# Kernel optimization log

Measured on AMD Instinct MI355X. Metric: run time of the kernel, lower is better.

## Reference

```python
import jax, jax.numpy as jnp
import numpy as np

N_NODES = 50000
N_EDGES = 640000
IN_CH, HID, OUT_CH = 128, 256, 3


def setup_inputs() -> dict:
    key = jax.random.key(0)
    ks = jax.random.split(key, 6)
    x = jax.random.normal(ks[0], (N_NODES, IN_CH), dtype=jnp.float32)
    edge_index = jax.random.randint(ks[1], (2, N_EDGES), 0, N_NODES, dtype=jnp.int64)
    # Glorot-ish scaling for weights
    Wl0 = jax.random.normal(ks[2], (IN_CH, HID), dtype=jnp.float32) / np.sqrt(IN_CH)
    bl0 = jnp.zeros((HID,), dtype=jnp.float32)
    Wr0 = jax.random.normal(ks[3], (IN_CH, HID), dtype=jnp.float32) / np.sqrt(IN_CH)
    Wl1 = jax.random.normal(ks[4], (HID, OUT_CH), dtype=jnp.float32) / np.sqrt(HID)
    bl1 = jnp.zeros((OUT_CH,), dtype=jnp.float32)
    Wr1 = jax.random.normal(ks[5], (HID, OUT_CH), dtype=jnp.float32) / np.sqrt(HID)
    return {"x": x, "edge_index": edge_index, "Wl0": Wl0, "bl0": bl0, "Wr0": Wr0,
            "Wl1": Wl1, "bl1": bl1, "Wr1": Wr1}


def _sage_conv(x, src, dst, Wl, bl, Wr, num_nodes):
    # mean aggregation of source features into destination nodes
    msg_sum = jax.ops.segment_sum(x[src], dst, num_segments=num_nodes)  # [N, d_in]
    deg = jax.ops.segment_sum(jnp.ones((src.shape[0],), x.dtype), dst, num_segments=num_nodes)
    mean = msg_sum / jnp.maximum(deg, 1.0)[:, None]
    # PyG SAGEConv: lin_l(aggr) + lin_r(x_self); lin_l carries the bias
    return mean @ Wl + bl + x @ Wr


def reference(x, edge_index, Wl0, bl0, Wr0, Wl1, bl1, Wr1):
    src, dst = edge_index[0], edge_index[1]
    h = _sage_conv(x, src, dst, Wl0, bl0, Wr0, N_NODES)
    h = jax.nn.relu(h)
    # dropout is identity in eval mode (training=False)
    return _sage_conv(h, src, dst, Wl1, bl1, Wr1, N_NODES)
```

## Files before the change

### kernel.cpp

```cpp
#include <hip/hip_runtime.h>

#define NN 50000
#define NNP 50048
#define NE 640000
#define IC 128
#define HC 256
#define OC 3

#define TOBF16_BLOCKS (NN * IC / 4 / 256)
#define WPACK_BLOCKS  32
#define ZERO_BLOCKS   ((NN + 1 + 255) / 256)

typedef __attribute__((ext_vector_type(8))) short short8;
typedef __attribute__((ext_vector_type(4))) float f32x4;

__device__ __forceinline__ unsigned short f2bf(float f) {
    unsigned int u = __float_as_uint(f);
    unsigned int r = u + 0x7FFFu + ((u >> 16) & 1u);
    return (unsigned short)(r >> 16);
}
__device__ __forceinline__ float bflo(unsigned int v) { return __uint_as_float(v << 16); }
__device__ __forceinline__ float bfhi(unsigned int v) { return __uint_as_float(v & 0xffff0000u); }

__global__ __launch_bounds__(256) void k_prep(const float* __restrict__ x,
                                              const float* __restrict__ Wl0,
                                              const float* __restrict__ Wr0,
                                              unsigned short* __restrict__ Ab,
                                              unsigned short* __restrict__ Bp,
                                              int* __restrict__ degi) {
    int b = blockIdx.x;
    int t = threadIdx.x;
    if (b < TOBF16_BLOCKS) {
        int i = b * 256 + t;
        int n = i >> 5;
        int c = (i & 31) * 4;
        float4 v = ((const float4*)x)[i];
        ushort4 o;
        o.x = f2bf(v.x); o.y = f2bf(v.y); o.z = f2bf(v.z); o.w = f2bf(v.w);
        *(ushort4*)&Ab[(size_t)n * 256 + 128 + c] = o;
    } else if (b < TOBF16_BLOCKS + WPACK_BLOCKS) {
        int tt = (b - TOBF16_BLOCKS) * 256 + t;
        int l = tt & 63;
        int nt = (tt >> 6) & 15;
        int kt = tt >> 10;
        int n = nt * 16 + (l & 15);
        int kbase = kt * 32 + (l >> 4) * 8;
        unsigned short o[8];
        #pragma unroll
        for (int e = 0; e < 8; ++e) {
            int k = kbase + e;
            float w = (k < IC) ? Wl0[k * HC + n] : Wr0[(k - IC) * HC + n];
            o[e] = f2bf(w);
        }
        #pragma unroll
        for (int e = 0; e < 8; ++e) Bp[(size_t)tt * 8 + e] = o[e];
    } else {
        int idx = (b - TOBF16_BLOCKS - WPACK_BLOCKS) * 256 + t;
        if (idx <= NN) degi[idx] = 0;
    }
}

__global__ __launch_bounds__(256) void k_deg(const int* __restrict__ ei,
                                             int* __restrict__ degi,
                                             int* __restrict__ pos) {
    int e = blockIdx.x * blockDim.x + threadIdx.x;
    if (e >= NE) return;
    pos[e] = atomicAdd(&degi[ei[NE + e]], 1);
}

__global__ __launch_bounds__(256) void k_ticket(const int* __restrict__ degi,
                                                int* __restrict__ counter,
                                                int* __restrict__ rowstart) {
    int n = blockIdx.x * blockDim.x + threadIdx.x;
    if (n >= NN) return;
    rowstart[n] = atomicAdd(counter, degi[n]);
}

__global__ __launch_bounds__(256) void k_fill(const int* __restrict__ ei,
                                              const int* __restrict__ rowstart,
                                              const int* __restrict__ pos,
                                              int* __restrict__ csr) {
    int e = blockIdx.x * blockDim.x + threadIdx.x;
    if (e >= NE) return;
    int src = ei[e];
    int dst = ei[NE + e];
    csr[rowstart[dst] + pos[e]] = src;
}

__global__ __launch_bounds__(256) void k_agg(const int* __restrict__ rowstart,
                                             const int* __restrict__ degi,
                                             const int* __restrict__ csr,
                                             unsigned short* __restrict__ Ab) {
    int wid = (blockIdx.x * blockDim.x + threadIdx.x) >> 6;
    int lane = threadIdx.x & 63;
    if (wid >= NN) return;
    int deg = degi[wid];
    int beg = rowstart[wid];
    int sg = lane >> 4;
    int s  = lane & 15;
    const uint4* base = (const uint4*)Ab;

    float a[8] = {0.f, 0.f, 0.f, 0.f, 0.f, 0.f, 0.f, 0.f};
    for (int j = beg + sg; j < beg + deg; j += 4) {
        int src = csr[j];
        uint4 v = base[(size_t)src * 32 + 16 + s];
        a[0] += bflo(v.x); a[1] += bfhi(v.x);
        a[2] += bflo(v.y); a[3] += bfhi(v.y);
        a[4] += bflo(v.z); a[5] += bfhi(v.z);
        a[6] += bflo(v.w); a[7] += bfhi(v.w);
    }
    #pragma unroll
    for (int m = 16; m <= 32; m <<= 1)
        #pragma unroll
        for (int i = 0; i < 8; ++i) a[i] += __shfl_xor(a[i], m);

    if (sg == 0) {
        float inv = 1.0f / fmaxf((float)deg, 1.0f);
        uint4 o;
        o.x = ((unsigned int)f2bf(a[1] * inv) << 16) | f2bf(a[0] * inv);
        o.y = ((unsigned int)f2bf(a[3] * inv) << 16) | f2bf(a[2] * inv);
        o.z = ((unsigned int)f2bf(a[5] * inv) << 16) | f2bf(a[4] * inv);
        o.w = ((unsigned int)f2bf(a[7] * inv) << 16) | f2bf(a[6] * inv);
        ((uint4*)Ab)[(size_t)wid * 32 + s] = o;
    }
}

__global__ __launch_bounds__(256) void k_gemm(const unsigned short* __restrict__ Ab,
                                              const unsigned short* __restrict__ Bp,
                                              const float* __restrict__ bl0,
                                              const float* __restrict__ Wl1,
                                              const float* __restrict__ Wr1,
                                              float* __restrict__ g,
                                              float* __restrict__ r) {
    __shared__ float4 Bs[2048];
    __shared__ float wl1s[HC][3];
    __shared__ float wr1s[HC][3];
    __shared__ float bls[HC];

    int t = threadIdx.x;
    for (int i = t; i < HC * 3; i += 256) {
        wl1s[i / 3][i % 3] = Wl1[i];
        wr1s[i / 3][i % 3] = Wr1[i];
    }
    for (int i = t; i < HC; i += 256) bls[i] = bl0[i];

    int w = t >> 6, l = t & 63;
    int n0 = blockIdx.x * 64 + w * 16;

    f32x4 acc[16];
    #pragma unroll
    for (int i = 0; i < 16; ++i) acc[i] = (f32x4){0.f, 0.f, 0.f, 0.f};

    const short8* A8 = (const short8*)Ab + ((size_t)(n0 + (l & 15)) * 32 + (l >> 4));

    for (int q = 0; q < 4; ++q) {
        __syncthreads();
        const float4* gsrc = (const float4*)(Bp + (size_t)q * 16384);
        #pragma unroll
        for (int i = 0; i < 8; ++i)
            Bs[i * 256 + t] = gsrc[i * 256 + t];
        __syncthreads();
        #pragma unroll
        for (int j = 0; j < 2; ++j) {
            int kt = q * 2 + j;
            short8 af = A8[kt * 4];
            const short8* B8 = (const short8*)Bs + (j * 1024 + l);
            #pragma unroll
            for (int nt = 0; nt < 16; ++nt) {
                short8 bf = B8[nt * 64];
                acc[nt] = __builtin_amdgcn_mfma_f32_16x16x32_bf16(af, bf, acc[nt], 0, 0, 0);
            }
        }
    }

    float pl[4][3] = {{0.f}}, pr[4][3] = {{0.f}};
    #pragma unroll
    for (int nt = 0; nt < 16; ++nt) {
        int col = nt * 16 + (l & 15);
        float b = bls[col];
        #pragma unroll
        for (int e = 0; e < 4; ++e) {
            float h = fmaxf(acc[nt][e] + b, 0.0f);
            #pragma unroll
            for (int j = 0; j < 3; ++j) {
                pl[e][j] = fmaf(h, wl1s[col][j], pl[e][j]);
                pr[e][j] = fmaf(h, wr1s[col][j], pr[e][j]);
            }
        }
    }
    #pragma unroll
    for (int m = 1; m <= 8; m <<= 1) {
        #pragma unroll
        for (int e = 0; e < 4; ++e)
            #pragma unroll
            for (int j = 0; j < 3; ++j) {
                pl[e][j] += __shfl_xor(pl[e][j], m);
                pr[e][j] += __shfl_xor(pr[e][j], m);
            }
    }
    if ((l & 15) == 0) {
        #pragma unroll
        for (int e = 0; e < 4; ++e) {
            int node = n0 + (l >> 4) * 4 + e;
            if (node < NN) {
                #pragma unroll
                for (int j = 0; j < 3; ++j) {
                    g[node * 3 + j] = pl[e][j];
                    r[node * 3 + j] = pr[e][j];
                }
            }
        }
    }
}

__global__ __launch_bounds__(256) void k_out(const int* __restrict__ rowstart,
                                             const int* __restrict__ degi,
                                             const int* __restrict__ csr,
                                             const float* __restrict__ g,
                                             const float* __restrict__ r,
                                             const float* __restrict__ bl1,
                                             float* __restrict__ out) {
    int tid = blockIdx.x * 256 + threadIdx.x;
    int n = tid >> 3;
    int sl = tid & 7;
    if (n >= NN) return;
    int deg = degi[n];
    int beg = rowstart[n];
    float s0 = 0.f, s1 = 0.f, s2 = 0.f;
    for (int j = beg + sl; j < beg + deg; j += 8) {
        int src = csr[j];
        s0 += g[src * 3 + 0];
        s1 += g[src * 3 + 1];
        s2 += g[src * 3 + 2];
    }
    #pragma unroll
    for (int m = 1; m < 8; m <<= 1) {
        s0 += __shfl_xor(s0, m);
        s1 += __shfl_xor(s1, m);
        s2 += __shfl_xor(s2, m);
    }
    if (sl == 0) {
        float inv = 1.0f / fmaxf((float)deg, 1.0f);
        out[n * 3 + 0] = s0 * inv + bl1[0] + r[n * 3 + 0];
        out[n * 3 + 1] = s1 * inv + bl1[1] + r[n * 3 + 1];
        out[n * 3 + 2] = s2 * inv + bl1[2] + r[n * 3 + 2];
    }
}

extern "C" void kernel_launch(void* const* d_in, const int* in_sizes, int n_in,
                              void* d_out, int out_size, void* d_ws, size_t ws_size,
                              hipStream_t stream) {
    const float* x   = (const float*)d_in[0];
    const int*   ei  = (const int*)d_in[1];
    const float* Wl0 = (const float*)d_in[2];
    const float* bl0 = (const float*)d_in[3];
    const float* Wr0 = (const float*)d_in[4];
    const float* Wl1 = (const float*)d_in[5];
    const float* bl1 = (const float*)d_in[6];
    const float* Wr1 = (const float*)d_in[7];
    float* out = (float*)d_out;

    char* ws = (char*)d_ws;
    int*            degi     = (int*)(ws);
    int*            rowstart = (int*)(ws + 200064);
    int*            pos      = (int*)(ws + 400128);
    int*            csr      = (int*)(ws + 2960128);
    unsigned short* Ab       = (unsigned short*)(ws + 5520128);
    unsigned short* Bp       = (unsigned short*)(ws + 31144704);
    float*          g        = (float*)(ws + 31275776);
    float*          r        = (float*)(ws + 31875840);

    int* counter = degi + NN;

    k_prep  <<<TOBF16_BLOCKS + WPACK_BLOCKS + ZERO_BLOCKS, 256, 0, stream>>>(x, Wl0, Wr0, Ab, Bp, degi);
    k_deg   <<<(NE + 255) / 256, 256, 0, stream>>>(ei, degi, pos);
    k_ticket<<<(NN + 255) / 256, 256, 0, stream>>>(degi, counter, rowstart);
    k_fill  <<<(NE + 255) / 256, 256, 0, stream>>>(ei, rowstart, pos, csr);
    k_agg   <<<(NN * 64 + 255) / 256, 256, 0, stream>>>(rowstart, degi, csr, Ab);
    k_gemm  <<<(NN + 63) / 64, 256, 0, stream>>>(Ab, Bp, bl0, Wl1, Wr1, g, r);
    k_out   <<<(NN * 8 + 255) / 256, 256, 0, stream>>>(rowstart, degi, csr, g, r, bl1, out);
}
```

Measured before the change: 125.4 us.

## Split GEMM over hidden halves with full-K B tile in LDS and atomic epilogue

The layer-0 GEMM now launches a 2D grid in which each block handles 256 rows and one half (128 columns) of the hidden dimension. It loads the entire K extent of its B slice into shared memory once, with no inner syncs, and each wave computes two 16-row tiles that reuse each B fragment. Because the two column halves produce partial sums of the tiny second-layer projection, g and r are zero-initialised in the prep kernel and accumulated with float atomics. This trades per-block B reloads and syncs for atomic traffic, twice the reads of the A operand, and a larger padded Ab buffer.

Measured after the change: 137.6 us. 9.8% more time.

```diff
diff --git a/kernel.cpp b/kernel.cpp
--- a/kernel.cpp
+++ b/kernel.cpp
@@ -1,7 +1,7 @@
 #include <hip/hip_runtime.h>
 
 #define NN 50000
-#define NNP 50048
+#define NNP 50176
 #define NE 640000
 #define IC 128
 #define HC 256
@@ -10,6 +10,7 @@
 #define TOBF16_BLOCKS (NN * IC / 4 / 256)
 #define WPACK_BLOCKS  32
 #define ZERO_BLOCKS   ((NN + 1 + 255) / 256)
+#define GR0_BLOCKS    293
 
 typedef __attribute__((ext_vector_type(8))) short short8;
 typedef __attribute__((ext_vector_type(4))) float f32x4;
@@ -27,7 +28,8 @@
                                               const float* __restrict__ Wr0,
                                               unsigned short* __restrict__ Ab,
                                               unsigned short* __restrict__ Bp,
-                                              int* __restrict__ degi) {
+                                              int* __restrict__ degi,
+                                              float4* __restrict__ gr) {
     int b = blockIdx.x;
     int t = threadIdx.x;
     if (b < TOBF16_BLOCKS) {
@@ -54,9 +56,12 @@
         }
         #pragma unroll
         for (int e = 0; e < 8; ++e) Bp[(size_t)tt * 8 + e] = o[e];
-    } else {
+    } else if (b < TOBF16_BLOCKS + WPACK_BLOCKS + ZERO_BLOCKS) {
         int idx = (b - TOBF16_BLOCKS - WPACK_BLOCKS) * 256 + t;
         if (idx <= NN) degi[idx] = 0;
+    } else {
+        int idx = (b - TOBF16_BLOCKS - WPACK_BLOCKS - ZERO_BLOCKS) * 256 + t;
+        if (idx < 75008) gr[idx] = make_float4(0.f, 0.f, 0.f, 0.f);
     }
 }
 
@@ -125,92 +130,95 @@
     }
 }
 
-__global__ __launch_bounds__(256) void k_gemm(const unsigned short* __restrict__ Ab,
+#define EPILOGUE(ACC, ROWOFF)                                                     \
+    do {                                                                          \
+        float pl[4][3] = {{0.f}}, pr[4][3] = {{0.f}};                             \
+        _Pragma("unroll") for (int nt = 0; nt < 8; ++nt) {                        \
+            int c = nt * 16 + (l & 15);                                           \
+            float bcol = bls[c];                                                  \
+            _Pragma("unroll") for (int e = 0; e < 4; ++e) {                       \
+                float hv = fmaxf(ACC[nt][e] + bcol, 0.0f);                        \
+                _Pragma("unroll") for (int j = 0; j < 3; ++j) {                   \
+                    pl[e][j] = fmaf(hv, wl1s[c][j], pl[e][j]);                    \
+                    pr[e][j] = fmaf(hv, wr1s[c][j], pr[e][j]);                    \
+                }                                                                 \
+            }                                                                     \
+        }                                                                         \
+        _Pragma("unroll") for (int m = 1; m <= 8; m <<= 1)                        \
+            _Pragma("unroll") for (int e = 0; e < 4; ++e)                         \
+                _Pragma("unroll") for (int j = 0; j < 3; ++j) {                   \
+                    pl[e][j] += __shfl_xor(pl[e][j], m);                          \
+                    pr[e][j] += __shfl_xor(pr[e][j], m);                          \
+                }                                                                 \
+        if ((l & 15) == 0) {                                                      \
+            _Pragma("unroll") for (int e = 0; e < 4; ++e) {                       \
+                int node = r0 + (ROWOFF) + (l >> 4) * 4 + e;                      \
+                if (node < NN) {                                                  \
+                    _Pragma("unroll") for (int j = 0; j < 3; ++j) {               \
+                        unsafeAtomicAdd(&g[node * 3 + j], pl[e][j]);              \
+                        unsafeAtomicAdd(&r[node * 3 + j], pr[e][j]);              \
+                    }                                                             \
+                }                                                                 \
+            }                                                                     \
+        }                                                                         \
+    } while (0)
+
+__global__ __launch_bounds__(512) void k_gemm(const unsigned short* __restrict__ Ab,
                                               const unsigned short* __restrict__ Bp,
                                               const float* __restrict__ bl0,
                                               const float* __restrict__ Wl1,
                                               const float* __restrict__ Wr1,
                                               float* __restrict__ g,
                                               float* __restrict__ r) {
-    __shared__ float4 Bs[2048];
-    __shared__ float wl1s[HC][3];
-    __shared__ float wr1s[HC][3];
-    __shared__ float bls[HC];
+    __shared__ float4 Bs[4096];
+    __shared__ float wl1s[128][3];
+    __shared__ float wr1s[128][3];
+    __shared__ float bls[128];
 
     int t = threadIdx.x;
-    for (int i = t; i < HC * 3; i += 256) {
-        wl1s[i / 3][i % 3] = Wl1[i];
-        wr1s[i / 3][i % 3] = Wr1[i];
-    }
-    for (int i = t; i < HC; i += 256) bls[i] = bl0[i];
+    int h = blockIdx.y;
+    int nbase = blockIdx.x * 256;
+
+    const float4* Bp4 = (const float4*)Bp;
+    #pragma unroll
+    for (int i = 0; i < 8; ++i) {
+        int q = i * 512 + t;
+        int kt = q >> 9, ntl = (q >> 6) & 7, lq = q & 63;
+        Bs[q] = Bp4[(kt * 16 + h * 8 + ntl) * 64 + lq];
+    }
+    for (int i = t; i < 128 * 3; i += 512) {
+        int c = i / 3, j = i % 3;
+        int col = h * 128 + c;
+        wl1s[c][j] = Wl1[col * 3 + j];
+        wr1s[c][j] = Wr1[col * 3 + j];
+    }
+    if (t < 128) bls[t] = bl0[h * 128 + t];
+    __syncthreads();
 
     int w = t >> 6, l = t & 63;
-    int n0 = blockIdx.x * 64 + w * 16;
-
-    f32x4 acc[16];
-    #pragma unroll
-    for (int i = 0; i < 16; ++i) acc[i] = (f32x4){0.f, 0.f, 0.f, 0.f};
-
-    const short8* A8 = (const short8*)Ab + ((size_t)(n0 + (l & 15)) * 32 + (l >> 4));
-
-    for (int q = 0; q < 4; ++q) {
-        __syncthreads();
-        const float4* gsrc = (const float4*)(Bp + (size_t)q * 16384);
-        #pragma unroll
-        for (int i = 0; i < 8; ++i)
-            Bs[i * 256 + t] = gsrc[i * 256 + t];
-        __syncthreads();
-        #pragma unroll
-        for (int j = 0; j < 2; ++j) {
-            int kt = q * 2 + j;
-            short8 af = A8[kt * 4];
-            const short8* B8 = (const short8*)Bs + (j * 1024 + l);
-            #pragma unroll
-            for (int nt = 0; nt < 16; ++nt) {
-                short8 bf = B8[nt * 64];
-                acc[nt] = __builtin_amdgcn_mfma_f32_16x16x32_bf16(af, bf, acc[nt], 0, 0, 0);
-            }
+    int r0 = nbase + w * 32;
+    const short8* A8a = (const short8*)Ab + ((size_t)(r0 + (l & 15)) * 32 + (l >> 4));
+    const short8* A8b = A8a + 16 * 32;
+
+    f32x4 acc0[8], acc1[8];
+    #pragma unroll
+    for (int i = 0; i < 8; ++i) { acc0[i] = (f32x4){0.f,0.f,0.f,0.f}; acc1[i] = (f32x4){0.f,0.f,0.f,0.f}; }
+
+    const short8* B8 = (const short8*)Bs + l;
+    #pragma unroll
+    for (int kt = 0; kt < 8; ++kt) {
+        short8 af0 = A8a[kt * 4];
+        short8 af1 = A8b[kt * 4];
+        #pragma unroll
+        for (int nt = 0; nt < 8; ++nt) {
+            short8 bf = B8[(kt * 8 + nt) * 64];
+            acc0[nt] = __builtin_amdgcn_mfma_f32_16x16x32_bf16(af0, bf, acc0[nt], 0, 0, 0);
+            acc1[nt] = __builtin_amdgcn_mfma_f32_16x16x32_bf16(af1, bf, acc1[nt], 0, 0, 0);
         }
     }
 
-    float pl[4][3] = {{0.f}}, pr[4][3] = {{0.f}};
-    #pragma unroll
-    for (int nt = 0; nt < 16; ++nt) {
-        int col = nt * 16 + (l & 15);
-        float b = bls[col];
-        #pragma unroll
-        for (int e = 0; e < 4; ++e) {
-            float h = fmaxf(acc[nt][e] + b, 0.0f);
-            #pragma unroll
-            for (int j = 0; j < 3; ++j) {
-                pl[e][j] = fmaf(h, wl1s[col][j], pl[e][j]);
-                pr[e][j] = fmaf(h, wr1s[col][j], pr[e][j]);
-            }
-        }
-    }
-    #pragma unroll
-    for (int m = 1; m <= 8; m <<= 1) {
-        #pragma unroll
-        for (int e = 0; e < 4; ++e)
-            #pragma unroll
-            for (int j = 0; j < 3; ++j) {
-                pl[e][j] += __shfl_xor(pl[e][j], m);
-                pr[e][j] += __shfl_xor(pr[e][j], m);
-            }
-    }
-    if ((l & 15) == 0) {
-        #pragma unroll
-        for (int e = 0; e < 4; ++e) {
-            int node = n0 + (l >> 4) * 4 + e;
-            if (node < NN) {
-                #pragma unroll
-                for (int j = 0; j < 3; ++j) {
-                    g[node * 3 + j] = pl[e][j];
-                    r[node * 3 + j] = pr[e][j];
-                }
-            }
-        }
-    }
+    EPILOGUE(acc0, 0);
+    EPILOGUE(acc1, 16);
 }
 
 __global__ __launch_bounds__(256) void k_out(const int* __restrict__ rowstart,
@@ -266,17 +274,18 @@
     int*            pos      = (int*)(ws + 400128);
     int*            csr      = (int*)(ws + 2960128);
     unsigned short* Ab       = (unsigned short*)(ws + 5520128);
-    unsigned short* Bp       = (unsigned short*)(ws + 31144704);
-    float*          g        = (float*)(ws + 31275776);
-    float*          r        = (float*)(ws + 31875840);
+    unsigned short* Bp       = (unsigned short*)(ws + 31210240);
+    float*          g        = (float*)(ws + 31341312);
+    float*          r        = (float*)(ws + 31941376);
 
     int* counter = degi + NN;
 
-    k_prep  <<<TOBF16_BLOCKS + WPACK_BLOCKS + ZERO_BLOCKS, 256, 0, stream>>>(x, Wl0, Wr0, Ab, Bp, degi);
+    k_prep  <<<TOBF16_BLOCKS + WPACK_BLOCKS + ZERO_BLOCKS + GR0_BLOCKS, 256, 0, stream>>>
+            (x, Wl0, Wr0, Ab, Bp, degi, (float4*)g);
     k_deg   <<<(NE + 255) / 256, 256, 0, stream>>>(ei, degi, pos);
     k_ticket<<<(NN + 255) / 256, 256, 0, stream>>>(degi, counter, rowstart);
     k_fill  <<<(NE + 255) / 256, 256, 0, stream>>>(ei, rowstart, pos, csr);
     k_agg   <<<(NN * 64 + 255) / 256, 256, 0, stream>>>(rowstart, degi, csr, Ab);
-    k_gemm  <<<(NN + 63) / 64, 256, 0, stream>>>(Ab, Bp, bl0, Wl1, Wr1, g, r);
+    k_gemm  <<<dim3(NNP / 256, 2), 512, 0, stream>>>(Ab, Bp, bl0, Wl1, Wr1, g, r);
     k_out   <<<(NN * 8 + 255) / 256, 256, 0, stream>>>(rowstart, degi, csr, g, r, bl1, out);
 }
```
